# Optimization experiments

Measured on AMD Instinct MI355X. Metric: run time of the kernel, lower is better.

The kernel has to match this reference:

```python
import jax, jax.numpy as jnp
import numpy as np

N_NODES = 8192
N_EDGES = 65536
D_MODEL = 64
D_INNER = 128
D_STATE = 16
DT_RANK = 4
LAYER_NUM = 3
TAU = 0.01


def _unif(key, shape, fan_out):
    stdv = 1.0 / np.sqrt(fan_out)
    return jax.random.uniform(key, shape, jnp.float32, -stdv, stdv)


def setup_inputs() -> dict:
    key = jax.random.key(0)
    ks = jax.random.split(key, 12)
    x = jax.random.normal(ks[0], (N_NODES, D_MODEL), jnp.float32)
    edge_index = jax.random.randint(ks[1], (2, N_EDGES), 0, N_NODES, jnp.int64)
    in_proj_w = _unif(ks[2], (D_MODEL, 2 * D_INNER), 2 * D_INNER)
    x_proj_w = _unif(ks[3], (D_INNER, DT_RANK + 2 * D_STATE), DT_RANK + 2 * D_STATE)
    dt_proj_w = _unif(ks[4], (DT_RANK, D_INNER), D_INNER)
    out_proj_w = _unif(ks[5], (D_INNER, D_MODEL), D_MODEL)
    A_log = jnp.log(jnp.broadcast_to(jnp.arange(1, D_STATE + 1, dtype=jnp.float32)[None, :], (D_INNER, D_STATE)))
    D = jnp.ones((D_INNER,), jnp.float32)
    in_act_w = _unif(ks[6], (D_INNER, 2), 2)
    in_act_b = _unif(ks[7], (2,), 2)
    out_act_w = _unif(ks[8], (D_INNER, 2), 2)
    out_act_b = _unif(ks[9], (2,), 2)
    return {"x": x, "in_proj_w": in_proj_w, "x_proj_w": x_proj_w, "dt_proj_w": dt_proj_w,
            "A_log": A_log, "D": D, "out_proj_w": out_proj_w,
            "in_act_w": in_act_w, "in_act_b": in_act_b, "out_act_w": out_act_w, "out_act_b": out_act_b,
            "edge_index": edge_index, "layer_num": LAYER_NUM}


def _norm_adj(row, col, w, n_nodes):
    # SparseTensor(...).set_diag() adds diag value 1; symmetric deg^-1/2 renorm
    deg = jax.ops.segment_sum(w, row, num_segments=n_nodes) + 1.0
    dinv = jnp.where(deg > 0, deg ** -0.5, 0.0)
    return dinv[row] * w * dinv[col], dinv * dinv  # off-diag edge weights, diag weights


def _spmm(row, col, ew, dw, x, n_nodes):
    # adj @ x with adj = edges(ew) + diag(dw); x: [N, F]
    return jax.ops.segment_sum(ew[:, None] * x[col], row, num_segments=n_nodes) + dw[:, None] * x


def _gumbel_hard(logits, key, tau):
    g = jax.random.gumbel(key, logits.shape, logits.dtype)
    y = jax.nn.softmax((logits + g) / tau, axis=-1)
    hard = jax.nn.one_hot(jnp.argmax(y, axis=-1), logits.shape[-1], dtype=y.dtype)
    return hard + y - jax.lax.stop_gradient(y)


def reference(x, in_proj_w, x_proj_w, dt_proj_w, A_log, D, out_proj_w,
              in_act_w, in_act_b, out_act_w, out_act_b, edge_index, layer_num):
    n_nodes, d_model = x.shape
    d_inner = dt_proj_w.shape[1]
    n = A_log.shape[1]
    dt_rank = dt_proj_w.shape[0]
    row, col = edge_index[0], edge_index[1]

    xl = jnp.broadcast_to(x[:, None, :], (n_nodes, layer_num, d_model))  # [N,L,d_model]
    x_and_res = xl @ in_proj_w                                           # [N,L,2*d_inner]
    xs, res = jnp.split(x_and_res, 2, axis=-1)
    xs = jax.nn.relu(xs)                                                 # u in scan

    A = -jnp.exp(A_log)                                                  # [d_inner, n]
    x_dbl = xs @ x_proj_w                                                # [N,L,dt_rank+2n]
    delta = jax.nn.softplus(x_dbl[..., :dt_rank] @ dt_proj_w)            # [N,L,d_inner]
    B = x_dbl[..., dt_rank:dt_rank + n]                                  # [N,L,n]
    C = x_dbl[..., dt_rank + n:]                                         # [N,L,n]

    deltaA = jnp.exp(jnp.einsum('bld,dn->bldn', delta, A))               # [N,L,d_inner,n]
    deltaB_u = jnp.einsum('bld,bln->bldn', delta * xs, B)                # [N,L,d_inner,n]

    # initial adjacency: unit-weight edges, sym-normalized with self loops
    ew, dw = _norm_adj(row, col, jnp.ones((row.shape[0],), xs.dtype), n_nodes)
    state = jnp.zeros((n_nodes, d_inner, n), xs.dtype)
    gkey = jax.random.key(42)
    ys = []
    for i in range(layer_num):  # small fixed number of GCN/SSM steps
        state = deltaA[:, i] * state + deltaB_u[:, i]
        y = jnp.einsum('bdn,bn->bd', state, C[:, i])                     # [N,d_inner]
        flat = _spmm(row, col, ew, dw, state.reshape(n_nodes, d_inner * n), n_nodes)
        state = flat.reshape(n_nodes, d_inner, n)
        in_p = _gumbel_hard(y @ in_act_w + in_act_b, jax.random.fold_in(gkey, 2 * i), TAU)
        out_p = _gumbel_hard(y @ out_act_w + out_act_b, jax.random.fold_in(gkey, 2 * i + 1), TAU)
        w = in_p[col, 0] * out_p[row, 0]  # keep_in_prob[v] * keep_out_prob[u]
        ew, dw = _norm_adj(row, col, w, n_nodes)
        ys.append(y)

    y = jnp.stack(ys, axis=1) + xs * D                                   # [N,L,d_inner]
    y = y * jax.nn.relu(res)
    out = y @ out_proj_w                                                 # [N,L,d_model]
    return out[:, -1, :]
```

## Files before the change

kernel.cpp:

```cpp
#include <hip/hip_runtime.h>
#include <cstdint>

#define NN 8192
#define NE 65536
#define G 8
#define CAP 64

typedef _Float16 h8 __attribute__((ext_vector_type(8)));
typedef _Float16 h2 __attribute__((ext_vector_type(2)));

__host__ __device__ inline void tf2x32(uint32_t k0, uint32_t k1,
                                       uint32_t x0, uint32_t x1,
                                       uint32_t& r0, uint32_t& r1) {
  uint32_t ks2 = k0 ^ k1 ^ 0x1BD11BDAu;
  x0 += k0; x1 += k1;
#define TF_ROT(x,d) (((x)<<(d))|((x)>>(32-(d))))
#define TF_R4(ra,rb,rc,rd) \
  x0+=x1; x1=TF_ROT(x1,ra); x1^=x0; \
  x0+=x1; x1=TF_ROT(x1,rb); x1^=x0; \
  x0+=x1; x1=TF_ROT(x1,rc); x1^=x0; \
  x0+=x1; x1=TF_ROT(x1,rd); x1^=x0;
  TF_R4(13,15,26,6)  x0+=k1;  x1+=ks2+1u;
  TF_R4(17,29,16,24) x0+=ks2; x1+=k0+2u;
  TF_R4(13,15,26,6)  x0+=k0;  x1+=k1+3u;
  TF_R4(17,29,16,24) x0+=k1;  x1+=ks2+4u;
  TF_R4(13,15,26,6)  x0+=ks2; x1+=k0+5u;
  r0=x0; r1=x1;
#undef TF_R4
#undef TF_ROT
}

__device__ inline float gumbel32(uint32_t k0, uint32_t k1, uint32_t idx) {
  uint32_t a, b;
  tf2x32(k0, k1, 0u, idx, a, b);
  uint32_t bits = a ^ b;
  float f = __uint_as_float((bits >> 9) | 0x3f800000u) - 1.0f;
  float u = (f > 0.0f) ? f : 1.17549435e-38f;
  return -logf(-logf(u));
}

__global__ __launch_bounds__(256) void k_nodeprep(
    const float* __restrict__ x, const float* __restrict__ ipw,
    const float* __restrict__ xpw, const float* __restrict__ dtw,
    const float* __restrict__ iaw, const float* __restrict__ iab,
    const float* __restrict__ oaw, const float* __restrict__ oab,
    const float* __restrict__ alog, const float* __restrict__ wout,
    const int* __restrict__ ei,
    uint32_t ki0, uint32_t ki1, uint32_t ko0, uint32_t ko1,
    float* __restrict__ xs, float* __restrict__ rres,
    float* __restrict__ delta, _Float16* __restrict__ dxh2,
    float* __restrict__ Bm, _Float16* __restrict__ Bh,
    float* __restrict__ Cm,
    float* __restrict__ inp, float* __restrict__ outp,
    float* __restrict__ Amat, _Float16* __restrict__ woh,
    int* __restrict__ cnt, int* __restrict__ csr_col) {
  __shared__ float sx[G][64];
  __shared__ float sxs[G][128];
  __shared__ float sdbl[G][36];
  __shared__ float sdx[G][128];
  int t = threadIdx.x;
  int b0 = blockIdx.x * G;
  if (t < 64) {
    int e = blockIdx.x * 64 + t;
    int v = ei[e];
    int pos = atomicAdd(&cnt[v], 1);
    if (pos < CAP) csr_col[(v<<6) + pos] = ei[NE + e];
  }
  {
    int i = blockIdx.x * 8 + (t & 7);
    if (t < 8) woh[i] = (_Float16)wout[i];
  }
  if (blockIdx.x == 0) {
    for (int i = t; i < 2048; i += 256) Amat[i] = -expf(alog[i]);
  }
  for (int i = t; i < G*64; i += 256) sx[i>>6][i&63] = x[b0*64 + i];
  __syncthreads();
  float acc[G];
#pragma unroll
  for (int g = 0; g < G; g++) acc[g] = 0.f;
  for (int k = 0; k < 64; k++) {
    float w = ipw[k*256 + t];
#pragma unroll
    for (int g = 0; g < G; g++) acc[g] += sx[g][k] * w;
  }
  if (t < 128) {
#pragma unroll
    for (int g = 0; g < G; g++) {
      float v = fmaxf(acc[g], 0.f);
      sxs[g][t] = v;
      xs[(size_t)(b0+g)*128 + t] = v;
    }
  } else {
    int j = t - 128;
#pragma unroll
    for (int g = 0; g < G; g++) rres[(size_t)(b0+g)*128 + j] = fmaxf(acc[g], 0.f);
  }
  __syncthreads();
  for (int idx = t; idx < G*36; idx += 256) {
    int g = idx / 36, c = idx % 36;
    float a = 0.f;
    for (int d = 0; d < 128; d++) a += sxs[g][d] * xpw[d*36 + c];
    sdbl[g][c] = a;
    if (c >= 4 && c < 20) {
      Bm[(b0+g)*16 + (c-4)] = a;
      Bh[(b0+g)*16 + (c-4)] = (_Float16)a;
    } else if (c >= 20)    Cm[(b0+g)*16 + (c-20)] = a;
  }
  __syncthreads();
  {
    int d = t & 127, hi = t >> 7;
#pragma unroll
    for (int gg = 0; gg < G/2; gg++) {
      int g = hi*(G/2) + gg;
      int b = b0 + g;
      float dt = sdbl[g][0]*dtw[d]     + sdbl[g][1]*dtw[128+d]
               + sdbl[g][2]*dtw[256+d] + sdbl[g][3]*dtw[384+d];
      float dv = fmaxf(dt, 0.f) + log1pf(expf(-fabsf(dt)));
      delta[(size_t)b*128 + d] = dv;
      sdx[g][d] = dv * sxs[g][d];
    }
  }
  __syncthreads();
  for (int i = t; i < G*64; i += 256) {
    int g = i >> 6, d = i & 63;
    h2 pk;
    pk.x = (_Float16)sdx[g][d];
    pk.y = (_Float16)sdx[g][d + 64];
    ((h2*)(dxh2 + ((size_t)(b0+g) << 7)))[d] = pk;
  }
  int wid = t >> 6, lane = t & 63;
#pragma unroll
  for (int s = 0; s < 2; s++) {
    int g = wid*2 + s;
    int b = b0 + g;
    float da = sdx[g][lane], db = sdx[g][lane + 64];
    float4 pr;
    pr.x = da*iaw[2*lane]   + db*iaw[2*(lane+64)];
    pr.y = da*iaw[2*lane+1] + db*iaw[2*(lane+64)+1];
    pr.z = da*oaw[2*lane]   + db*oaw[2*(lane+64)];
    pr.w = da*oaw[2*lane+1] + db*oaw[2*(lane+64)+1];
    for (int off = 32; off >= 1; off >>= 1) {
      pr.x += __shfl_down(pr.x, off);
      pr.y += __shfl_down(pr.y, off);
      pr.z += __shfl_down(pr.z, off);
      pr.w += __shfl_down(pr.w, off);
    }
    if (lane == 0) {
      float BC = 0.f;
      for (int n = 0; n < 16; n++) BC += sdbl[g][4+n] * sdbl[g][20+n];
      float li0 = BC*pr.x + iab[0], li1 = BC*pr.y + iab[1];
      float lo0 = BC*pr.z + oab[0], lo1 = BC*pr.w + oab[1];
      uint32_t L0 = 2u*(uint32_t)b, L1 = L0 + 1u;
      inp[b]  = (li0 + gumbel32(ki0, ki1, L0) >= li1 + gumbel32(ki0, ki1, L1)) ? 1.0f : 0.0f;
      outp[b] = (lo0 + gumbel32(ko0, ko1, L0) >= lo1 + gumbel32(ko0, ko1, L1)) ? 1.0f : 0.0f;
    }
  }
}

__global__ __launch_bounds__(256) void k_spmm0f(
    const int* __restrict__ cnt, const int* __restrict__ csr_col,
    const float* __restrict__ inp, const float* __restrict__ outp,
    const float* __restrict__ delta, const _Float16* __restrict__ dxh2,
    const float* __restrict__ Bm, const _Float16* __restrict__ Bh,
    const float* __restrict__ Cm, const float* __restrict__ Amat,
    _Float16* __restrict__ s_out, float* __restrict__ dinv1,
    float* __restrict__ y2p) {
  __shared__ int   sc[2][CAP];
  __shared__ float scoef[2][CAP];
  __shared__ float sdegs[2];
  int t = threadIdx.x, half = t >> 7, tid2 = t & 127;
  int v = (blockIdx.x << 1) + half;
  int deg = min(cnt[v], CAP);
  if (tid2 < 64) {
    float g = 0.f;
    if (tid2 < deg) {
      int c = csr_col[(v<<6) + tid2];
      sc[half][tid2] = c;
      scoef[half][tid2] = 1.0f / sqrtf((float)min(cnt[c], CAP) + 1.0f);
      g = inp[c];
    }
    for (int off = 32; off >= 1; off >>= 1) g += __shfl_down(g, off);
    if (tid2 == 0) sdegs[half] = g;
  }
  __syncthreads();
  int d0 = tid2 >> 1, d1 = d0 + 64, nq = tid2 & 1;
  float dv = 1.0f / sqrtf((float)deg + 1.0f);
  const float4* BmV = (const float4*)(Bm + ((size_t)v << 4));
  float4 Bv0 = BmV[nq*2], Bv1 = BmV[nq*2+1];
  h2 pkv = ((const h2*)(dxh2 + ((size_t)v << 7)))[d0];
  float dx0 = (float)pkv.x, dx1 = (float)pkv.y;
  float dw = dv * dv;
  float c0 = dw * dx0, c1 = dw * dx1;
  float4 a0l = {c0*Bv0.x, c0*Bv0.y, c0*Bv0.z, c0*Bv0.w};
  float4 a0h = {c0*Bv1.x, c0*Bv1.y, c0*Bv1.z, c0*Bv1.w};
  float4 a1l = {c1*Bv0.x, c1*Bv0.y, c1*Bv0.z, c1*Bv0.w};
  float4 a1h = {c1*Bv1.x, c1*Bv1.y, c1*Bv1.z, c1*Bv1.w};
#pragma unroll 4
  for (int j = 0; j < deg; j++) {
    int c = sc[half][j];
    float coef = dv * scoef[half][j];
    h2 pk = ((const h2*)(dxh2 + ((size_t)c << 7)))[d0];
    h8 Bp = ((const h8*)(Bh + ((size_t)c << 4)))[nq];
    float e0 = coef * (float)pk.x;
    float e1 = coef * (float)pk.y;
    float b0f = (float)Bp[0], b1f = (float)Bp[1], b2f = (float)Bp[2], b3f = (float)Bp[3];
    float b4f = (float)Bp[4], b5f = (float)Bp[5], b6f = (float)Bp[6], b7f = (float)Bp[7];
    a0l.x += e0*b0f; a0l.y += e0*b1f; a0l.z += e0*b2f; a0l.w += e0*b3f;
    a0h.x += e0*b4f; a0h.y += e0*b5f; a0h.z += e0*b6f; a0h.w += e0*b7f;
    a1l.x += e1*b0f; a1l.y += e1*b1f; a1l.z += e1*b2f; a1l.w += e1*b3f;
    a1h.x += e1*b4f; a1h.y += e1*b5f; a1h.z += e1*b6f; a1h.w += e1*b7f;
  }
  float de0 = delta[v*128 + d0], de1 = delta[v*128 + d1];
  const float4* A0p = (const float4*)(Amat + (d0 << 4));
  const float4* A1p = (const float4*)(Amat + (d1 << 4));
  float4 A00 = A0p[nq*2], A01 = A0p[nq*2+1];
  float4 A10 = A1p[nq*2], A11 = A1p[nq*2+1];
  float4 E0l, E0h, E1l, E1h;
  E0l.x = expf(de0*A00.x); E0l.y = expf(de0*A00.y); E0l.z = expf(de0*A00.z); E0l.w = expf(de0*A00.w);
  E0h.x = expf(de0*A01.x); E0h.y = expf(de0*A01.y); E0h.z = expf(de0*A01.z); E0h.w = expf(de0*A01.w);
  E1l.x = expf(de1*A10.x); E1l.y = expf(de1*A10.y); E1l.z = expf(de1*A10.z); E1l.w = expf(de1*A10.w);
  E1h.x = expf(de1*A11.x); E1h.y = expf(de1*A11.y); E1h.z = expf(de1*A11.z); E1h.w = expf(de1*A11.w);
  float4 s0l, s0h, s1l, s1h;
  s0l.x = E0l.x*a0l.x + dx0*Bv0.x; s0l.y = E0l.y*a0l.y + dx0*Bv0.y;
  s0l.z = E0l.z*a0l.z + dx0*Bv0.z; s0l.w = E0l.w*a0l.w + dx0*Bv0.w;
  s0h.x = E0h.x*a0h.x + dx0*Bv1.x; s0h.y = E0h.y*a0h.y + dx0*Bv1.y;
  s0h.z = E0h.z*a0h.z + dx0*Bv1.z; s0h.w = E0h.w*a0h.w + dx0*Bv1.w;
  s1l.x = E1l.x*a1l.x + dx1*Bv0.x; s1l.y = E1l.y*a1l.y + dx1*Bv0.y;
  s1l.z = E1l.z*a1l.z + dx1*Bv0.z; s1l.w = E1l.w*a1l.w + dx1*Bv0.w;
  s1h.x = E1h.x*a1h.x + dx1*Bv1.x; s1h.y = E1h.y*a1h.y + dx1*Bv1.y;
  s1h.z = E1h.z*a1h.z + dx1*Bv1.z; s1h.w = E1h.w*a1h.w + dx1*Bv1.w;
  if (inp[v] != 0.f) {
    h8* op = (h8*)(s_out + ((size_t)v << 11));
    h8 p0, p1;
    p0[0]=(_Float16)s0l.x; p0[1]=(_Float16)s0l.y; p0[2]=(_Float16)s0l.z; p0[3]=(_Float16)s0l.w;
    p0[4]=(_Float16)s0h.x; p0[5]=(_Float16)s0h.y; p0[6]=(_Float16)s0h.z; p0[7]=(_Float16)s0h.w;
    p1[0]=(_Float16)s1l.x; p1[1]=(_Float16)s1l.y; p1[2]=(_Float16)s1l.z; p1[3]=(_Float16)s1l.w;
    p1[4]=(_Float16)s1h.x; p1[5]=(_Float16)s1h.y; p1[6]=(_Float16)s1h.z; p1[7]=(_Float16)s1h.w;
    op[d0*2 + nq] = p0;
    op[d0*2 + 128 + nq] = p1;
  }
  float degs = sdegs[half];
  float d1v = 1.0f / sqrtf(outp[v]*degs + 1.0f);
  if (tid2 == 0) dinv1[v] = d1v;
  float dw1 = d1v * d1v;
  const float4* CmV = (const float4*)(Cm + ((size_t)v << 4));
  float4 Cv0 = CmV[nq*2], Cv1 = CmV[nq*2+1];
  float BvC = Bv0.x*Cv0.x + Bv0.y*Cv0.y + Bv0.z*Cv0.z + Bv0.w*Cv0.w
            + Bv1.x*Cv1.x + Bv1.y*Cv1.y + Bv1.z*Cv1.z + Bv1.w*Cv1.w;
  float y0p = dw1*(E0l.x*s0l.x*Cv0.x + E0l.y*s0l.y*Cv0.y + E0l.z*s0l.z*Cv0.z + E0l.w*s0l.w*Cv0.w
                 + E0h.x*s0h.x*Cv1.x + E0h.y*s0h.y*Cv1.y + E0h.z*s0h.z*Cv1.z + E0h.w*s0h.w*Cv1.w)
            + dx0*BvC;
  float y1p = dw1*(E1l.x*s1l.x*Cv0.x + E1l.y*s1l.y*Cv0.y + E1l.z*s1l.z*Cv0.z + E1l.w*s1l.w*Cv0.w
                 + E1h.x*s1h.x*Cv1.x + E1h.y*s1h.y*Cv1.y + E1h.z*s1h.z*Cv1.z + E1h.w*s1h.w*Cv1.w)
            + dx1*BvC;
  y0p += __shfl_xor(y0p, 1);
  y1p += __shfl_xor(y1p, 1);
  if (nq == 0) {
    y2p[v*128 + d0] = y0p;
    y2p[v*128 + d1] = y1p;
  }
}

__global__ __launch_bounds__(256) void k_spmm1fo(
    const int* __restrict__ cnt, const int* __restrict__ csr_col,
    const float* __restrict__ dinv1,
    const float* __restrict__ inp, const float* __restrict__ outp,
    const float* __restrict__ delta,
    const float* __restrict__ Cm, const float* __restrict__ Amat,
    const _Float16* __restrict__ s_in, const float* __restrict__ y2p,
    const float* __restrict__ xs, const float* __restrict__ rres,
    const float* __restrict__ Dv, const _Float16* __restrict__ woh,
    float* __restrict__ out) {
  __shared__ int   sc[2][CAP];
  __shared__ float scoef[2][CAP];
  __shared__ int   snact[2];
  __shared__ float ty[2][128];
  __shared__ float sproj[2][64];
  __shared__ _Float16 swout[8192];
  int t = threadIdx.x, half = t >> 7, tid2 = t & 127;
  int v = (blockIdx.x << 1) + half;
  {
    const uint4* src = (const uint4*)woh;
    uint4* dst = (uint4*)swout;
    for (int i = t; i < 1024; i += 256) dst[i] = src[i];
  }
  if (tid2 == 0) snact[half] = 0;
  if (tid2 < 64) {
    int deg = (outp[v] != 0.f) ? min(cnt[v], CAP) : 0;
    if (tid2 < deg) {
      int c = csr_col[(v<<6) + tid2];
      if (inp[c] != 0.f) {
        int p = atomicAdd(&snact[half], 1);
        sc[half][p] = c; scoef[half][p] = dinv1[c];
      }
    }
  }
  __syncthreads();
  int nact = snact[half];
  int d0 = tid2 >> 1, d1 = d0 + 64, nq = tid2 & 1;
  float dv = dinv1[v];
  float4 a0l = {0.f,0.f,0.f,0.f}, a0h = {0.f,0.f,0.f,0.f};
  float4 a1l = {0.f,0.f,0.f,0.f}, a1h = {0.f,0.f,0.f,0.f};
#pragma unroll 4
  for (int j = 0; j < nact; j++) {
    int c = sc[half][j];
    float coef = dv * scoef[half][j];
    const h8* rp = (const h8*)(s_in + ((size_t)c << 11));
    h8 n0 = rp[d0*2 + nq], n1 = rp[d0*2 + 128 + nq];
    a0l.x += coef*(float)n0[0]; a0l.y += coef*(float)n0[1];
    a0l.z += coef*(float)n0[2]; a0l.w += coef*(float)n0[3];
    a0h.x += coef*(float)n0[4]; a0h.y += coef*(float)n0[5];
    a0h.z += coef*(float)n0[6]; a0h.w += coef*(float)n0[7];
    a1l.x += coef*(float)n1[0]; a1l.y += coef*(float)n1[1];
    a1l.z += coef*(float)n1[2]; a1l.w += coef*(float)n1[3];
    a1h.x += coef*(float)n1[4]; a1h.y += coef*(float)n1[5];
    a1h.z += coef*(float)n1[6]; a1h.w += coef*(float)n1[7];
  }
  float y0g = 0.f, y1g = 0.f;
  if (nact > 0) {
    float de0 = delta[v*128 + d0], de1 = delta[v*128 + d1];
    const float4* A0p = (const float4*)(Amat + (d0 << 4));
    const float4* A1p = (const float4*)(Amat + (d1 << 4));
    float4 A00 = A0p[nq*2], A01 = A0p[nq*2+1];
    float4 A10 = A1p[nq*2], A11 = A1p[nq*2+1];
    const float4* CmV = (const float4*)(Cm + ((size_t)v << 4));
    float4 Cv0 = CmV[nq*2], Cv1 = CmV[nq*2+1];
    y0g = expf(de0*A00.x)*a0l.x*Cv0.x + expf(de0*A00.y)*a0l.y*Cv0.y
        + expf(de0*A00.z)*a0l.z*Cv0.z + expf(de0*A00.w)*a0l.w*Cv0.w
        + expf(de0*A01.x)*a0h.x*Cv1.x + expf(de0*A01.y)*a0h.y*Cv1.y
        + expf(de0*A01.z)*a0h.z*Cv1.z + expf(de0*A01.w)*a0h.w*Cv1.w;
    y1g = expf(de1*A10.x)*a1l.x*Cv0.x + expf(de1*A10.y)*a1l.y*Cv0.y
        + expf(de1*A10.z)*a1l.z*Cv0.z + expf(de1*A10.w)*a1l.w*Cv0.w
        + expf(de1*A11.x)*a1h.x*Cv1.x + expf(de1*A11.y)*a1h.y*Cv1.y
        + expf(de1*A11.z)*a1h.z*Cv1.z + expf(de1*A11.w)*a1h.w*Cv1.w;
  }
  y0g += __shfl_xor(y0g, 1);
  y1g += __shfl_xor(y1g, 1);
  if (nq == 0) {
    float yA = y0g + y2p[v*128 + d0];
    float yB = y1g + y2p[v*128 + d1];
    ty[half][d0] = (yA + xs[v*128 + d0]*Dv[d0]) * rres[v*128 + d0];
    ty[half][d1] = (yB + xs[v*128 + d1]*Dv[d1]) * rres[v*128 + d1];
  }
  __syncthreads();
  int oc = tid2 & 63, ks = tid2 >> 6;
  const float* typ = ty[half];
  float acc = 0.f;
  for (int d = ks*64; d < ks*64 + 64; d++) acc += typ[d] * (float)swout[d*64 + oc];
  if (ks == 1) sproj[half][oc] = acc;
  __syncthreads();
  if (ks == 0) out[v*64 + oc] = acc + sproj[half][oc];
}

extern "C" void kernel_launch(void* const* d_in, const int* in_sizes, int n_in,
                              void* d_out, int out_size, void* d_ws, size_t ws_size,
                              hipStream_t stream) {
  const float* x    = (const float*)d_in[0];
  const float* ipw  = (const float*)d_in[1];
  const float* xpw  = (const float*)d_in[2];
  const float* dtw  = (const float*)d_in[3];
  const float* alog = (const float*)d_in[4];
  const float* Dv   = (const float*)d_in[5];
  const float* wout = (const float*)d_in[6];
  const float* iaw  = (const float*)d_in[7];
  const float* iab  = (const float*)d_in[8];
  const float* oaw  = (const float*)d_in[9];
  const float* oab  = (const float*)d_in[10];
  const int*   ei   = (const int*)d_in[11];
  (void)in_sizes; (void)n_in; (void)out_size; (void)ws_size;

  float* W = (float*)d_ws;
  size_t o = 0;
  float* xs    = W + o; o += (size_t)NN*128;
  float* rres  = W + o; o += (size_t)NN*128;
  float* delta = W + o; o += (size_t)NN*128;
  float* y2p   = W + o; o += (size_t)NN*128;
  float* Bm    = W + o; o += (size_t)NN*16;
  float* Cm    = W + o; o += (size_t)NN*16;
  float* Amat  = W + o; o += 2048;
  float* dinv1 = W + o; o += NN;
  float* inp   = W + o; o += NN;
  float* outp  = W + o; o += NN;
  _Float16* dxh2 = (_Float16*)(W + o); o += (size_t)NN*64;
  _Float16* Bh   = (_Float16*)(W + o); o += (size_t)NN*8;
  _Float16* woh  = (_Float16*)(W + o); o += 4096;
  _Float16* stA  = (_Float16*)(W + o); o += (size_t)NN*1024;
  int* cnt     = (int*)(W + o);
  int* csr_col = cnt + NN;

  uint32_t ki0, ki1, ko0, ko1;
  tf2x32(0u, 42u, 0u, 0u, ki0, ki1);
  tf2x32(0u, 42u, 0u, 1u, ko0, ko1);

  hipMemsetAsync(cnt, 0, NN*sizeof(int), stream);

  k_nodeprep<<<NN/G, 256, 0, stream>>>(x, ipw, xpw, dtw, iaw, iab, oaw, oab,
                                       alog, wout, ei, ki0, ki1, ko0, ko1,
                                       xs, rres, delta, dxh2, Bm, Bh, Cm,
                                       inp, outp, Amat, woh, cnt, csr_col);

  k_spmm0f<<<NN/2, 256, 0, stream>>>(cnt, csr_col, inp, outp,
                                     delta, dxh2, Bm, Bh, Cm, Amat,
                                     stA, dinv1, y2p);

  k_spmm1fo<<<NN/2, 256, 0, stream>>>(cnt, csr_col, dinv1, inp, outp,
                                      delta, Cm, Amat, stA, y2p,
                                      xs, rres, Dv, woh, (float*)d_out);
}
```

Baseline: 169.4 us.

## Split neighbor loop across thread pairs, one node per block, transposed swizzled out-proj weights

Both SpMM kernels now assign one node per 256-thread block instead of two. Each (d,nq) slot is covered by two threads that take alternating neighbors and combine their partial sums with shuffles, which shortens the serial gather loop and doubles the thread count per node. The output projection reads a transposed fp16 weight matrix from XOR-swizzled shared memory using h8 vector loads, split across four k-slices. Gumbel noise is now computed in parallel across four lanes rather than serially in lane 0. The cost is more blocks, so the per-block copy of the weights into shared memory happens twice as often, plus extra shuffle work.

Measured after the change: 171.4 us. Within noise of the previous version (+1.2%).

```diff
diff --git a/kernel.cpp b/kernel.cpp
--- a/kernel.cpp
+++ b/kernel.cpp
@@ -52,7 +52,7 @@
     float* __restrict__ Bm, _Float16* __restrict__ Bh,
     float* __restrict__ Cm,
     float* __restrict__ inp, float* __restrict__ outp,
-    float* __restrict__ Amat, _Float16* __restrict__ woh,
+    float* __restrict__ Amat, _Float16* __restrict__ woT,
     int* __restrict__ cnt, int* __restrict__ csr_col) {
   __shared__ float sx[G][64];
   __shared__ float sxs[G][128];
@@ -68,7 +68,10 @@
   }
   {
     int i = blockIdx.x * 8 + (t & 7);
-    if (t < 8) woh[i] = (_Float16)wout[i];
+    if (t < 8) {
+      int d = i >> 6, oc = i & 63;
+      woT[oc*128 + d] = (_Float16)wout[i];
+    }
   }
   if (blockIdx.x == 0) {
     for (int i = t; i < 2048; i += 256) Amat[i] = -expf(alog[i]);
@@ -145,14 +148,21 @@
       pr.z += __shfl_down(pr.z, off);
       pr.w += __shfl_down(pr.w, off);
     }
+    float gsel = 0.f;
+    if (lane < 4) {
+      uint32_t kk0 = (lane < 2) ? ki0 : ko0;
+      uint32_t kk1 = (lane < 2) ? ki1 : ko1;
+      gsel = gumbel32(kk0, kk1, 2u*(uint32_t)b + (uint32_t)(lane & 1));
+    }
+    float g0 = __shfl(gsel, 0), g1 = __shfl(gsel, 1);
+    float g2 = __shfl(gsel, 2), g3 = __shfl(gsel, 3);
     if (lane == 0) {
       float BC = 0.f;
       for (int n = 0; n < 16; n++) BC += sdbl[g][4+n] * sdbl[g][20+n];
       float li0 = BC*pr.x + iab[0], li1 = BC*pr.y + iab[1];
       float lo0 = BC*pr.z + oab[0], lo1 = BC*pr.w + oab[1];
-      uint32_t L0 = 2u*(uint32_t)b, L1 = L0 + 1u;
-      inp[b]  = (li0 + gumbel32(ki0, ki1, L0) >= li1 + gumbel32(ki0, ki1, L1)) ? 1.0f : 0.0f;
-      outp[b] = (lo0 + gumbel32(ko0, ko1, L0) >= lo1 + gumbel32(ko0, ko1, L1)) ? 1.0f : 0.0f;
+      inp[b]  = (li0 + g0 >= li1 + g1) ? 1.0f : 0.0f;
+      outp[b] = (lo0 + g2 >= lo1 + g3) ? 1.0f : 0.0f;
     }
   }
 }
@@ -165,40 +175,36 @@
     const float* __restrict__ Cm, const float* __restrict__ Amat,
     _Float16* __restrict__ s_out, float* __restrict__ dinv1,
     float* __restrict__ y2p) {
-  __shared__ int   sc[2][CAP];
-  __shared__ float scoef[2][CAP];
-  __shared__ float sdegs[2];
-  int t = threadIdx.x, half = t >> 7, tid2 = t & 127;
-  int v = (blockIdx.x << 1) + half;
+  __shared__ int   sc[CAP];
+  __shared__ float scoef[CAP];
+  __shared__ float sdeg;
+  int t = threadIdx.x;
+  int v = blockIdx.x;
   int deg = min(cnt[v], CAP);
-  if (tid2 < 64) {
+  if (t < 64) {
     float g = 0.f;
-    if (tid2 < deg) {
-      int c = csr_col[(v<<6) + tid2];
-      sc[half][tid2] = c;
-      scoef[half][tid2] = 1.0f / sqrtf((float)min(cnt[c], CAP) + 1.0f);
+    if (t < deg) {
+      int c = csr_col[(v<<6) + t];
+      sc[t] = c;
+      scoef[t] = 1.0f / sqrtf((float)min(cnt[c], CAP) + 1.0f);
       g = inp[c];
     }
     for (int off = 32; off >= 1; off >>= 1) g += __shfl_down(g, off);
-    if (tid2 == 0) sdegs[half] = g;
-  }
-  __syncthreads();
-  int d0 = tid2 >> 1, d1 = d0 + 64, nq = tid2 & 1;
+    if (t == 0) sdeg = g;
+  }
+  __syncthreads();
+  int js = t & 1, nq = (t >> 1) & 1, d0 = t >> 2, d1 = d0 + 64;
   float dv = 1.0f / sqrtf((float)deg + 1.0f);
   const float4* BmV = (const float4*)(Bm + ((size_t)v << 4));
   float4 Bv0 = BmV[nq*2], Bv1 = BmV[nq*2+1];
   h2 pkv = ((const h2*)(dxh2 + ((size_t)v << 7)))[d0];
   float dx0 = (float)pkv.x, dx1 = (float)pkv.y;
-  float dw = dv * dv;
-  float c0 = dw * dx0, c1 = dw * dx1;
-  float4 a0l = {c0*Bv0.x, c0*Bv0.y, c0*Bv0.z, c0*Bv0.w};
-  float4 a0h = {c0*Bv1.x, c0*Bv1.y, c0*Bv1.z, c0*Bv1.w};
-  float4 a1l = {c1*Bv0.x, c1*Bv0.y, c1*Bv0.z, c1*Bv0.w};
-  float4 a1h = {c1*Bv1.x, c1*Bv1.y, c1*Bv1.z, c1*Bv1.w};
-#pragma unroll 4
-  for (int j = 0; j < deg; j++) {
-    int c = sc[half][j];
-    float coef = dv * scoef[half][j];
+  float4 a0l = {0.f,0.f,0.f,0.f}, a0h = {0.f,0.f,0.f,0.f};
+  float4 a1l = {0.f,0.f,0.f,0.f}, a1h = {0.f,0.f,0.f,0.f};
+#pragma unroll 2
+  for (int j = js; j < deg; j += 2) {
+    int c = sc[j];
+    float coef = dv * scoef[j];
     h2 pk = ((const h2*)(dxh2 + ((size_t)c << 7)))[d0];
     h8 Bp = ((const h8*)(Bh + ((size_t)c << 4)))[nq];
     float e0 = coef * (float)pk.x;
@@ -210,6 +216,20 @@
     a1l.x += e1*b0f; a1l.y += e1*b1f; a1l.z += e1*b2f; a1l.w += e1*b3f;
     a1h.x += e1*b4f; a1h.y += e1*b5f; a1h.z += e1*b6f; a1h.w += e1*b7f;
   }
+  a0l.x += __shfl_xor(a0l.x, 1); a0l.y += __shfl_xor(a0l.y, 1);
+  a0l.z += __shfl_xor(a0l.z, 1); a0l.w += __shfl_xor(a0l.w, 1);
+  a0h.x += __shfl_xor(a0h.x, 1); a0h.y += __shfl_xor(a0h.y, 1);
+  a0h.z += __shfl_xor(a0h.z, 1); a0h.w += __shfl_xor(a0h.w, 1);
+  a1l.x += __shfl_xor(a1l.x, 1); a1l.y += __shfl_xor(a1l.y, 1);
+  a1l.z += __shfl_xor(a1l.z, 1); a1l.w += __shfl_xor(a1l.w, 1);
+  a1h.x += __shfl_xor(a1h.x, 1); a1h.y += __shfl_xor(a1h.y, 1);
+  a1h.z += __shfl_xor(a1h.z, 1); a1h.w += __shfl_xor(a1h.w, 1);
+  float dw = dv * dv;
+  float c0 = dw * dx0, c1 = dw * dx1;
+  a0l.x += c0*Bv0.x; a0l.y += c0*Bv0.y; a0l.z += c0*Bv0.z; a0l.w += c0*Bv0.w;
+  a0h.x += c0*Bv1.x; a0h.y += c0*Bv1.y; a0h.z += c0*Bv1.z; a0h.w += c0*Bv1.w;
+  a1l.x += c1*Bv0.x; a1l.y += c1*Bv0.y; a1l.z += c1*Bv0.z; a1l.w += c1*Bv0.w;
+  a1h.x += c1*Bv1.x; a1h.y += c1*Bv1.y; a1h.z += c1*Bv1.z; a1h.w += c1*Bv1.w;
   float de0 = delta[v*128 + d0], de1 = delta[v*128 + d1];
   const float4* A0p = (const float4*)(Amat + (d0 << 4));
   const float4* A1p = (const float4*)(Amat + (d1 << 4));
@@ -229,7 +249,7 @@
   s1l.z = E1l.z*a1l.z + dx1*Bv0.z; s1l.w = E1l.w*a1l.w + dx1*Bv0.w;
   s1h.x = E1h.x*a1h.x + dx1*Bv1.x; s1h.y = E1h.y*a1h.y + dx1*Bv1.y;
   s1h.z = E1h.z*a1h.z + dx1*Bv1.z; s1h.w = E1h.w*a1h.w + dx1*Bv1.w;
-  if (inp[v] != 0.f) {
+  if (inp[v] != 0.f && js == 0) {
     h8* op = (h8*)(s_out + ((size_t)v << 11));
     h8 p0, p1;
     p0[0]=(_Float16)s0l.x; p0[1]=(_Float16)s0l.y; p0[2]=(_Float16)s0l.z; p0[3]=(_Float16)s0l.w;
@@ -239,9 +259,9 @@
     op[d0*2 + nq] = p0;
     op[d0*2 + 128 + nq] = p1;
   }
-  float degs = sdegs[half];
+  float degs = sdeg;
   float d1v = 1.0f / sqrtf(outp[v]*degs + 1.0f);
-  if (tid2 == 0) dinv1[v] = d1v;
+  if (t == 0) dinv1[v] = d1v;
   float dw1 = d1v * d1v;
   const float4* CmV = (const float4*)(Cm + ((size_t)v << 4));
   float4 Cv0 = CmV[nq*2], Cv1 = CmV[nq*2+1];
@@ -253,9 +273,9 @@
   float y1p = dw1*(E1l.x*s1l.x*Cv0.x + E1l.y*s1l.y*Cv0.y + E1l.z*s1l.z*Cv0.z + E1l.w*s1l.w*Cv0.w
                  + E1h.x*s1h.x*Cv1.x + E1h.y*s1h.y*Cv1.y + E1h.z*s1h.z*Cv1.z + E1h.w*s1h.w*Cv1.w)
             + dx1*BvC;
-  y0p += __shfl_xor(y0p, 1);
-  y1p += __shfl_xor(y1p, 1);
-  if (nq == 0) {
+  y0p += __shfl_xor(y0p, 2);
+  y1p += __shfl_xor(y1p, 2);
+  if ((t & 3) == 0) {
     y2p[v*128 + d0] = y0p;
     y2p[v*128 + d1] = y1p;
   }
@@ -269,42 +289,45 @@
     const float* __restrict__ Cm, const float* __restrict__ Amat,
     const _Float16* __restrict__ s_in, const float* __restrict__ y2p,
     const float* __restrict__ xs, const float* __restrict__ rres,
-    const float* __restrict__ Dv, const _Float16* __restrict__ woh,
+    const float* __restrict__ Dv, const _Float16* __restrict__ woT,
     float* __restrict__ out) {
-  __shared__ int   sc[2][CAP];
-  __shared__ float scoef[2][CAP];
-  __shared__ int   snact[2];
-  __shared__ float ty[2][128];
-  __shared__ float sproj[2][64];
-  __shared__ _Float16 swout[8192];
-  int t = threadIdx.x, half = t >> 7, tid2 = t & 127;
-  int v = (blockIdx.x << 1) + half;
+  __shared__ int   sc[CAP];
+  __shared__ float scoef[CAP];
+  __shared__ int   snact;
+  __shared__ float ty[128];
+  __shared__ float sproj[3][64];
+  __shared__ h8 swoT[1024];
+  int t = threadIdx.x;
+  int v = blockIdx.x;
   {
-    const uint4* src = (const uint4*)woh;
-    uint4* dst = (uint4*)swout;
-    for (int i = t; i < 1024; i += 256) dst[i] = src[i];
-  }
-  if (tid2 == 0) snact[half] = 0;
-  if (tid2 < 64) {
+    const uint4* src = (const uint4*)woT;
+    uint4* dst = (uint4*)swoT;
+    for (int i = t; i < 1024; i += 256) {
+      int oc = i >> 4, c = i & 15;
+      dst[(oc << 4) | (c ^ (oc & 7))] = src[i];
+    }
+  }
+  if (t == 0) snact = 0;
+  if (t < 64) {
     int deg = (outp[v] != 0.f) ? min(cnt[v], CAP) : 0;
-    if (tid2 < deg) {
-      int c = csr_col[(v<<6) + tid2];
+    if (t < deg) {
+      int c = csr_col[(v<<6) + t];
       if (inp[c] != 0.f) {
-        int p = atomicAdd(&snact[half], 1);
-        sc[half][p] = c; scoef[half][p] = dinv1[c];
+        int p = atomicAdd(&snact, 1);
+        sc[p] = c; scoef[p] = dinv1[c];
       }
     }
   }
   __syncthreads();
-  int nact = snact[half];
-  int d0 = tid2 >> 1, d1 = d0 + 64, nq = tid2 & 1;
+  int nact = snact;
+  int js = t & 1, nq = (t >> 1) & 1, d0 = t >> 2, d1 = d0 + 64;
   float dv = dinv1[v];
   float4 a0l = {0.f,0.f,0.f,0.f}, a0h = {0.f,0.f,0.f,0.f};
   float4 a1l = {0.f,0.f,0.f,0.f}, a1h = {0.f,0.f,0.f,0.f};
-#pragma unroll 4
-  for (int j = 0; j < nact; j++) {
-    int c = sc[half][j];
-    float coef = dv * scoef[half][j];
+#pragma unroll 2
+  for (int j = js; j < nact; j += 2) {
+    int c = sc[j];
+    float coef = dv * scoef[j];
     const h8* rp = (const h8*)(s_in + ((size_t)c << 11));
     h8 n0 = rp[d0*2 + nq], n1 = rp[d0*2 + 128 + nq];
     a0l.x += coef*(float)n0[0]; a0l.y += coef*(float)n0[1];
@@ -316,6 +339,14 @@
     a1h.x += coef*(float)n1[4]; a1h.y += coef*(float)n1[5];
     a1h.z += coef*(float)n1[6]; a1h.w += coef*(float)n1[7];
   }
+  a0l.x += __shfl_xor(a0l.x, 1); a0l.y += __shfl_xor(a0l.y, 1);
+  a0l.z += __shfl_xor(a0l.z, 1); a0l.w += __shfl_xor(a0l.w, 1);
+  a0h.x += __shfl_xor(a0h.x, 1); a0h.y += __shfl_xor(a0h.y, 1);
+  a0h.z += __shfl_xor(a0h.z, 1); a0h.w += __shfl_xor(a0h.w, 1);
+  a1l.x += __shfl_xor(a1l.x, 1); a1l.y += __shfl_xor(a1l.y, 1);
+  a1l.z += __shfl_xor(a1l.z, 1); a1l.w += __shfl_xor(a1l.w, 1);
+  a1h.x += __shfl_xor(a1h.x, 1); a1h.y += __shfl_xor(a1h.y, 1);
+  a1h.z += __shfl_xor(a1h.z, 1); a1h.w += __shfl_xor(a1h.w, 1);
   float y0g = 0.f, y1g = 0.f;
   if (nact > 0) {
     float de0 = delta[v*128 + d0], de1 = delta[v*128 + d1];
@@ -334,22 +365,29 @@
         + expf(de1*A11.x)*a1h.x*Cv1.x + expf(de1*A11.y)*a1h.y*Cv1.y
         + expf(de1*A11.z)*a1h.z*Cv1.z + expf(de1*A11.w)*a1h.w*Cv1.w;
   }
-  y0g += __shfl_xor(y0g, 1);
-  y1g += __shfl_xor(y1g, 1);
-  if (nq == 0) {
+  y0g += __shfl_xor(y0g, 2);
+  y1g += __shfl_xor(y1g, 2);
+  if ((t & 3) == 0) {
     float yA = y0g + y2p[v*128 + d0];
     float yB = y1g + y2p[v*128 + d1];
-    ty[half][d0] = (yA + xs[v*128 + d0]*Dv[d0]) * rres[v*128 + d0];
-    ty[half][d1] = (yB + xs[v*128 + d1]*Dv[d1]) * rres[v*128 + d1];
-  }
-  __syncthreads();
-  int oc = tid2 & 63, ks = tid2 >> 6;
-  const float* typ = ty[half];
+    ty[d0] = (yA + xs[v*128 + d0]*Dv[d0]) * rres[v*128 + d0];
+    ty[d1] = (yB + xs[v*128 + d1]*Dv[d1]) * rres[v*128 + d1];
+  }
+  __syncthreads();
+  int oc = t & 63, ks = t >> 6;
+  const float4* tyv = (const float4*)ty;
   float acc = 0.f;
-  for (int d = ks*64; d < ks*64 + 64; d++) acc += typ[d] * (float)swout[d*64 + oc];
-  if (ks == 1) sproj[half][oc] = acc;
-  __syncthreads();
-  if (ks == 0) out[v*64 + oc] = acc + sproj[half][oc];
+#pragma unroll
+  for (int i = 0; i < 4; i++) {
+    int c = (ks << 2) + i;
+    h8 wv = swoT[(oc << 4) | (c ^ (oc & 7))];
+    float4 t0 = tyv[c*2], t1 = tyv[c*2+1];
+    acc += t0.x*(float)wv[0] + t0.y*(float)wv[1] + t0.z*(float)wv[2] + t0.w*(float)wv[3]
+         + t1.x*(float)wv[4] + t1.y*(float)wv[5] + t1.z*(float)wv[6] + t1.w*(float)wv[7];
+  }
+  if (ks > 0) sproj[ks-1][oc] = acc;
+  __syncthreads();
+  if (ks == 0) out[v*64 + oc] = acc + sproj[0][oc] + sproj[1][oc] + sproj[2][oc];
 }
 
 extern "C" void kernel_launch(void* const* d_in, const int* in_sizes, int n_in,
@@ -383,7 +421,7 @@
   float* outp  = W + o; o += NN;
   _Float16* dxh2 = (_Float16*)(W + o); o += (size_t)NN*64;
   _Float16* Bh   = (_Float16*)(W + o); o += (size_t)NN*8;
-  _Float16* woh  = (_Float16*)(W + o); o += 4096;
+  _Float16* woT  = (_Float16*)(W + o); o += 4096;
   _Float16* stA  = (_Float16*)(W + o); o += (size_t)NN*1024;
   int* cnt     = (int*)(W + o);
   int* csr_col = cnt + NN;
@@ -397,13 +435,13 @@
   k_nodeprep<<<NN/G, 256, 0, stream>>>(x, ipw, xpw, dtw, iaw, iab, oaw, oab,
                                        alog, wout, ei, ki0, ki1, ko0, ko1,
                                        xs, rres, delta, dxh2, Bm, Bh, Cm,
-                                       inp, outp, Amat, woh, cnt, csr_col);
-
-  k_spmm0f<<<NN/2, 256, 0, stream>>>(cnt, csr_col, inp, outp,
-                                     delta, dxh2, Bm, Bh, Cm, Amat,
-                                     stA, dinv1, y2p);
-
-  k_spmm1fo<<<NN/2, 256, 0, stream>>>(cnt, csr_col, dinv1, inp, outp,
-                                      delta, Cm, Amat, stA, y2p,
-                                      xs, rres, Dv, woh, (float*)d_out);
-}
+                                       inp, outp, Amat, woT, cnt, csr_col);
+
+  k_spmm0f<<<NN, 256, 0, stream>>>(cnt, csr_col, inp, outp,
+                                   delta, dxh2, Bm, Bh, Cm, Amat,
+                                   stA, dinv1, y2p);
+
+  k_spmm1fo<<<NN, 256, 0, stream>>>(cnt, csr_col, dinv1, inp, outp,
+                                    delta, Cm, Amat, stA, y2p,
+                                    xs, rres, Dv, woT, (float*)d_out);
+}
```
